# Kernel optimization log

Hardware: AMD Instinct MI355X
Metric: run time of the kernel (lower is better)

The kernel has to match this reference:

```python
import jax, jax.numpy as jnp
import numpy as np

N = 50000      # nodes
E = 800000     # random edges (self-loops appended inside reference)
DIN = 128
DH = 32        # per-head hidden dim of layer 1
H = 8          # heads
DOUT = 32      # output dim (layer 2, concat=False)
NEG_SLOPE = 0.2


def segment_softmax(e, seg, num):
    # numerically stable softmax over variable-size segments (per-destination)
    m = jax.ops.segment_max(e, seg, num_segments=num)
    m = jnp.where(jnp.isfinite(m), m, jnp.zeros_like(m))
    ex = jnp.exp(e - m[seg])
    s = jax.ops.segment_sum(ex, seg, num_segments=num)
    return ex / (s[seg] + 1e-16)


def gatv2_conv(x, src, dst, Wl, Wr, att, bias, heads, dim, concat):
    n = x.shape[0]
    xl = (x @ Wl).reshape(n, heads, dim)   # source transform
    xr = (x @ Wr).reshape(n, heads, dim)   # target transform
    z = xl[src] + xr[dst]                  # [E, H, D] gather per edge
    z = jnp.where(z > 0, z, NEG_SLOPE * z) # LeakyReLU BEFORE attention vector (GATv2)
    e = jnp.einsum('ehd,hd->eh', z, att)   # attention logits [E, H]
    alpha = segment_softmax(e, dst, n)     # softmax over in-edges of each dst
    out = jax.ops.segment_sum(alpha[:, :, None] * xl[src], dst, num_segments=n)
    if concat:
        return out.reshape(n, heads * dim) + bias
    return out.mean(axis=1) + bias


def setup_inputs() -> dict:
    key = jax.random.key(0)
    ks = jax.random.split(key, 12)
    x = jax.random.normal(ks[0], (N, DIN), dtype=jnp.float32)
    edge_index = jax.random.randint(ks[1], (2, E), 0, N, dtype=jnp.int64)
    s = 0.05
    Wl1 = jax.random.normal(ks[2], (DIN, H * DH), dtype=jnp.float32) * s
    Wr1 = jax.random.normal(ks[3], (DIN, H * DH), dtype=jnp.float32) * s
    att1 = jax.random.normal(ks[4], (H, DH), dtype=jnp.float32) * s
    b1 = jnp.zeros((H * DH,), dtype=jnp.float32)
    Wl2 = jax.random.normal(ks[5], (H * DH, H * DOUT), dtype=jnp.float32) * s
    Wr2 = jax.random.normal(ks[6], (H * DH, H * DOUT), dtype=jnp.float32) * s
    att2 = jax.random.normal(ks[7], (H, DOUT), dtype=jnp.float32) * s
    b2 = jnp.zeros((DOUT,), dtype=jnp.float32)
    return {"x": x, "edge_index": edge_index, "Wl1": Wl1, "Wr1": Wr1,
            "att1": att1, "b1": b1, "Wl2": Wl2, "Wr2": Wr2,
            "att2": att2, "b2": b2}


def reference(x, edge_index, Wl1, Wr1, att1, b1, Wl2, Wr2, att2, b2):
    n = x.shape[0]
    loops = jnp.arange(n, dtype=edge_index.dtype)
    src = jnp.concatenate([edge_index[0], loops])  # PyG adds self-loops by default
    dst = jnp.concatenate([edge_index[1], loops])
    h = gatv2_conv(x, src, dst, Wl1, Wr1, att1, b1, H, DH, concat=True)
    h = jax.nn.elu(h)
    out = gatv2_conv(h, src, dst, Wl2, Wr2, att2, b2, H, DOUT, concat=False)
    return out
```

## Files before the change

kernel.cpp:

```cpp
#include <hip/hip_runtime.h>
#include <hip/hip_bf16.h>

typedef __hip_bfloat16 bf16;
typedef __attribute__((ext_vector_type(8))) short bf16x8;
typedef __attribute__((ext_vector_type(4))) float f32x4;

#define N_NODES 50000
#define E_RAW   800000
#define E_TOT   850000
#define H_HEADS 8
#define F_DIM   256
#define NB_SCAN 196

__device__ __forceinline__ float loadF(const void* p, size_t i, int f32) {
    return f32 ? ((const float*)p)[i] : __bfloat162float(((const bf16*)p)[i]);
}
__device__ __forceinline__ int loadI(const void* p, size_t i, int is32) {
    return is32 ? ((const int*)p)[i] : (int)((const long long*)p)[i];
}
__device__ __forceinline__ float uasf(unsigned u) { return __uint_as_float(u); }
__device__ __forceinline__ unsigned f2bfbits(float f) {
    unsigned u = __float_as_uint(f);
    return (u + 0x7fff + ((u >> 16) & 1)) >> 16;
}
__device__ __forceinline__ short f2bfs(float f) {
    unsigned u = __float_as_uint(f);
    return (short)((u + 0x7fff + ((u >> 16) & 1)) >> 16);
}

__global__ void detect_zero(const void* __restrict__ x, const void* __restrict__ ei,
                            int* __restrict__ flags, int* __restrict__ counts) {
    int gid = blockIdx.x * 256 + threadIdx.x;
    if (gid < N_NODES) counts[gid] = 0;
    if (blockIdx.x != 0) return;
    __shared__ int sf[2];
    int t = threadIdx.x;
    if (t < 2) sf[t] = 0;
    __syncthreads();
    const unsigned short* xs = (const unsigned short*)x;
    int f32 = 0;
    for (int i = t; i < 8192; i += 256) {
        unsigned e = (xs[i] >> 7) & 0xFF;
        if (e >= 134) f32 = 1;
    }
    const int* eii = (const int*)ei;
    int odd = 0;
    for (int i = t; i < 1024; i += 256)
        if (eii[2 * i + 1] != 0) odd = 1;
    if (f32) atomicOr(&sf[0], 1);
    if (odd) atomicOr(&sf[1], 1);
    __syncthreads();
    if (t < 2) flags[t] = sf[t];
}

__global__ void prep(const void* __restrict__ wl1, const void* __restrict__ wr1,
                     const void* __restrict__ wl2, const void* __restrict__ wr2,
                     const void* __restrict__ ei,
                     bf16* __restrict__ wb, int* __restrict__ counts,
                     unsigned short* __restrict__ rank,
                     const int* __restrict__ flags) {
    const int f32 = flags[0], is32 = flags[1];
    int gid = blockIdx.x * 256 + threadIdx.x;
    if (gid < E_TOT) {
        int d = (gid < E_RAW) ? loadI(ei, (size_t)E_RAW + gid, is32) : (gid - E_RAW);
        rank[gid] = (unsigned short)atomicAdd(&counts[d], 1);
    }
    for (size_t j = gid; j < 196608; j += (size_t)gridDim.x * 256) {
        const void* src; size_t off, base;
        int k, n;
        if (j < 65536) {
            int half = j >= 32768;
            off = j - (size_t)half * 32768;
            src = half ? wr1 : wl1;
            k = (int)(off >> 8); n = half * 256 + (int)(off & 255);
            base = 0;
        } else {
            size_t jj = j - 65536;
            int half = jj >= 65536;
            off = jj - (size_t)half * 65536;
            src = half ? wr2 : wl2;
            k = (int)(off >> 8); n = half * 256 + (int)(off & 255);
            base = 65536;
        }
        int kb = k >> 5, jo = k & 7;
        int lane = ((k >> 3) & 3) * 16 + (n & 15);
        int ctg = n >> 4;
        size_t dst = base + (((size_t)(kb * 32 + ctg) * 64 + lane) * 8 + jo);
        wb[dst] = __float2bfloat16(loadF(src, off, f32));
    }
}

__global__ void scan1(const int* __restrict__ counts, int* __restrict__ rp,
                      int* __restrict__ bsum) {
    __shared__ int sm[256];
    int b = blockIdx.x, t = threadIdx.x;
    int i = b * 256 + t;
    int v = (i < N_NODES) ? counts[i] : 0;
    sm[t] = v; __syncthreads();
    for (int off = 1; off < 256; off <<= 1) {
        int u = (t >= off) ? sm[t - off] : 0;
        __syncthreads();
        sm[t] += u;
        __syncthreads();
    }
    int incl = sm[t];
    if (i < N_NODES) rp[i] = incl - v;
    if (t == 255) bsum[b] = incl;
}

__global__ void scan2(int* __restrict__ bsum) {
    __shared__ int sm[256];
    int t = threadIdx.x;
    int v = (t < NB_SCAN) ? bsum[t] : 0;
    sm[t] = v; __syncthreads();
    for (int off = 1; off < 256; off <<= 1) {
        int u = (t >= off) ? sm[t - off] : 0;
        __syncthreads();
        sm[t] += u;
        __syncthreads();
    }
    if (t < NB_SCAN) bsum[t] = sm[t] - v;
}

__global__ void scan3(int* __restrict__ rp, const int* __restrict__ bsum) {
    int b = blockIdx.x, t = threadIdx.x;
    int i = b * 256 + t;
    if (i < N_NODES) rp[i] += bsum[b];
    if (i == 0) rp[N_NODES] = E_TOT;
}

__global__ void fill(const void* __restrict__ ei, const int* __restrict__ rp,
                     const unsigned short* __restrict__ rank,
                     int* __restrict__ srcs, const int* __restrict__ flags) {
    const int is32 = flags[1];
    int e = blockIdx.x * 256 + threadIdx.x;
    if (e >= E_TOT) return;
    int s, d;
    if (e < E_RAW) { s = loadI(ei, e, is32); d = loadI(ei, (size_t)E_RAW + e, is32); }
    else           { s = d = e - E_RAW; }
    srcs[rp[d] + rank[e]] = s;
}

__launch_bounds__(256)
__global__ void gemm_mfma(const void* __restrict__ A, const bf16* __restrict__ Wsw,
                          bf16* __restrict__ Cl, bf16* __restrict__ Cr,
                          int M, int K, int aDyn, const int* __restrict__ flags) {
    const int af32 = aDyn ? flags[0] : 0;
    const int tid = threadIdx.x;
    const int w = tid >> 6, lane = tid & 63, q = lane >> 4, l16 = lane & 15;
    const int bRow = blockIdx.x * 128 + (w >> 1) * 64;
    const int bCol = blockIdx.y * 128 + (w & 1) * 64;
    const int ctg0 = bCol >> 4;
    const short* Wp = (const short*)Wsw;
    const int nkb = K >> 5;
    int rows[4];
#pragma unroll
    for (int i = 0; i < 4; ++i) {
        int r = bRow + i * 16 + l16;
        rows[i] = r < M ? r : M - 1;
    }
    f32x4 acc[16] = {};
    for (int kb = 0; kb < nkb; ++kb) {
        bf16x8 a[4], b[4];
#pragma unroll
        for (int i = 0; i < 4; ++i) {
            if (!af32) {
                a[i] = *(const bf16x8*)((const short*)A + (size_t)rows[i] * K + q * 8 + kb * 32);
            } else {
                const float* Apf = (const float*)A + (size_t)rows[i] * K + q * 8 + kb * 32;
                float4 a0 = *(const float4*)(Apf);
                float4 a1 = *(const float4*)(Apf + 4);
                a[i][0] = f2bfs(a0.x); a[i][1] = f2bfs(a0.y);
                a[i][2] = f2bfs(a0.z); a[i][3] = f2bfs(a0.w);
                a[i][4] = f2bfs(a1.x); a[i][5] = f2bfs(a1.y);
                a[i][6] = f2bfs(a1.z); a[i][7] = f2bfs(a1.w);
            }
        }
#pragma unroll
        for (int j = 0; j < 4; ++j)
            b[j] = *(const bf16x8*)(Wp + ((size_t)(kb * 32 + ctg0 + j) * 64 + lane) * 8);
#pragma unroll
        for (int i = 0; i < 4; ++i)
#pragma unroll
            for (int j = 0; j < 4; ++j)
                acc[i * 4 + j] =
                    __builtin_amdgcn_mfma_f32_16x16x32_bf16(b[j], a[i], acc[i * 4 + j], 0, 0, 0);
    }
    unsigned short* C = (unsigned short*)(bCol < 256 ? Cl : Cr);
    const int cBase = (bCol < 256 ? bCol : bCol - 256) + q * 4;
#pragma unroll
    for (int i = 0; i < 4; ++i) {
        int row = bRow + i * 16 + l16;
        if (row < M) {
#pragma unroll
            for (int j = 0; j < 4; ++j) {
                f32x4 v = acc[i * 4 + j];
                uint2 o;
                o.x = f2bfbits(v[0]) | (f2bfbits(v[1]) << 16);
                o.y = f2bfbits(v[2]) | (f2bfbits(v[3]) << 16);
                *(uint2*)(C + (size_t)row * 256 + cBase + j * 16) = o;
            }
        }
    }
}

#define EDGE2(Q, PRED)                                                        \
    {                                                                         \
        float2 X0 = {uasf(Q.x << 16), uasf(Q.x & 0xffff0000u)};               \
        float2 X1 = {uasf(Q.y << 16), uasf(Q.y & 0xffff0000u)};               \
        float2 X2 = {uasf(Q.z << 16), uasf(Q.z & 0xffff0000u)};               \
        float2 X3 = {uasf(Q.w << 16), uasf(Q.w & 0xffff0000u)};               \
        float2 z0 = {X0.x + rv0.x, X0.y + rv0.y};                             \
        float2 z1 = {X1.x + rv1.x, X1.y + rv1.y};                             \
        float2 z2 = {X2.x + rv2.x, X2.y + rv2.y};                             \
        float2 z3 = {X3.x + rv3.x, X3.y + rv3.y};                             \
        z0.x = fmaxf(z0.x, 0.2f * z0.x); z0.y = fmaxf(z0.y, 0.2f * z0.y);     \
        z1.x = fmaxf(z1.x, 0.2f * z1.x); z1.y = fmaxf(z1.y, 0.2f * z1.y);     \
        z2.x = fmaxf(z2.x, 0.2f * z2.x); z2.y = fmaxf(z2.y, 0.2f * z2.y);     \
        z3.x = fmaxf(z3.x, 0.2f * z3.x); z3.y = fmaxf(z3.y, 0.2f * z3.y);     \
        float2 p2 = {z0.x * a0.x, z0.y * a0.y};                               \
        p2.x = fmaf(z1.x, a1.x, p2.x); p2.y = fmaf(z1.y, a1.y, p2.y);         \
        p2.x = fmaf(z2.x, a2.x, p2.x); p2.y = fmaf(z2.y, a2.y, p2.y);         \
        p2.x = fmaf(z3.x, a3.x, p2.x); p2.y = fmaf(z3.y, a3.y, p2.y);         \
        float p = p2.x + p2.y;                                                \
        p += __shfl_xor(p, 1); p += __shfl_xor(p, 2);                         \
        float wv = (PRED) ? __expf(p) : 0.f;                                  \
        den += wv;                                                            \
        n0.x = fmaf(wv, X0.x, n0.x); n0.y = fmaf(wv, X0.y, n0.y);             \
        n1.x = fmaf(wv, X1.x, n1.x); n1.y = fmaf(wv, X1.y, n1.y);             \
        n2.x = fmaf(wv, X2.x, n2.x); n2.y = fmaf(wv, X2.y, n2.y);             \
        n3.x = fmaf(wv, X3.x, n3.x); n3.y = fmaf(wv, X3.y, n3.y);             \
    }
__launch_bounds__(256)
__global__ void fused_attn(const int* __restrict__ rp, const int* __restrict__ srcs,
                           const bf16* __restrict__ xl, const bf16* __restrict__ xr,
                           const void* __restrict__ att, const void* __restrict__ bias,
                           void* __restrict__ outp, int mode,
                           const int* __restrict__ flags) {
    const int f32 = flags[0];
    const int tid = threadIdx.x, wid = tid >> 6, lane = tid & 63;
    const int sub = lane & 31;
    const int d = blockIdx.x * 8 + wid * 2 + (lane >> 5);

    const unsigned short* xru = (const unsigned short*)xr;
    uint4 xv = *(const uint4*)(xru + (size_t)d * 256 + sub * 8);
    float2 rv0 = {uasf(xv.x << 16), uasf(xv.x & 0xffff0000u)};
    float2 rv1 = {uasf(xv.y << 16), uasf(xv.y & 0xffff0000u)};
    float2 rv2 = {uasf(xv.z << 16), uasf(xv.z & 0xffff0000u)};
    float2 rv3 = {uasf(xv.w << 16), uasf(xv.w & 0xffff0000u)};
    float2 a0, a1, a2, a3;
    if (f32) {
        float4 t0 = *(const float4*)((const float*)att + sub * 8);
        float4 t1 = *(const float4*)((const float*)att + sub * 8 + 4);
        a0 = {t0.x, t0.y}; a1 = {t0.z, t0.w}; a2 = {t1.x, t1.y}; a3 = {t1.z, t1.w};
    } else {
        uint4 av = *(const uint4*)((const unsigned short*)att + sub * 8);
        a0 = {uasf(av.x << 16), uasf(av.x & 0xffff0000u)};
        a1 = {uasf(av.y << 16), uasf(av.y & 0xffff0000u)};
        a2 = {uasf(av.z << 16), uasf(av.z & 0xffff0000u)};
        a3 = {uasf(av.w << 16), uasf(av.w & 0xffff0000u)};
    }

    const int start = rp[d], cnt = rp[d + 1] - start;
    const int cnt1 = cnt - 1;
    int mA = __shfl(cnt, 0), mB = __shfl(cnt, 32);
    const int maxc = mA > mB ? mA : mB;
    const int* sp = srcs + start;
    const unsigned short* xlu = (const unsigned short*)xl + sub * 8;

    float den = 0.f;
    float2 n0 = {0,0}, n1 = {0,0}, n2 = {0,0}, n3 = {0,0};
    int i = 0;
    for (; i + 1 < maxc; i += 2) {
        int i0 = i < cnt1 ? i : cnt1;
        int i1 = i + 1 < cnt1 ? i + 1 : cnt1;
        int s0 = sp[i0], s1 = sp[i1];
        uint4 q0 = *(const uint4*)(xlu + (size_t)s0 * 256);
        uint4 q1 = *(const uint4*)(xlu + (size_t)s1 * 256);
        EDGE2(q0, i < cnt);
        EDGE2(q1, i + 1 < cnt);
    }
    if (i < maxc) {
        int i0 = i < cnt1 ? i : cnt1;
        int s0 = sp[i0];
        uint4 q0 = *(const uint4*)(xlu + (size_t)s0 * 256);
        EDGE2(q0, i < cnt);
    }
    float rd = 1.f / (den + 1e-16f);
    float v[8] = {n0.x * rd, n0.y * rd, n1.x * rd, n1.y * rd,
                  n2.x * rd, n2.y * rd, n3.x * rd, n3.y * rd};

    if (mode == 1) {
        float b[8];
        if (f32) {
            float4 t0 = *(const float4*)((const float*)bias + sub * 8);
            float4 t1 = *(const float4*)((const float*)bias + sub * 8 + 4);
            b[0]=t0.x; b[1]=t0.y; b[2]=t0.z; b[3]=t0.w;
            b[4]=t1.x; b[5]=t1.y; b[6]=t1.z; b[7]=t1.w;
        } else {
            uint4 bv = *(const uint4*)((const unsigned short*)bias + sub * 8);
            b[0]=uasf(bv.x<<16); b[1]=uasf(bv.x&0xffff0000u);
            b[2]=uasf(bv.y<<16); b[3]=uasf(bv.y&0xffff0000u);
            b[4]=uasf(bv.z<<16); b[5]=uasf(bv.z&0xffff0000u);
            b[6]=uasf(bv.w<<16); b[7]=uasf(bv.w&0xffff0000u);
        }
        uint4 o;
        unsigned oo[4];
#pragma unroll
        for (int k = 0; k < 4; ++k) {
            float u0 = v[2*k]   + b[2*k];
            float u1 = v[2*k+1] + b[2*k+1];
            u0 = u0 > 0.f ? u0 : expm1f(u0);
            u1 = u1 > 0.f ? u1 : expm1f(u1);
            oo[k] = f2bfbits(u0) | (f2bfbits(u1) << 16);
        }
        o.x = oo[0]; o.y = oo[1]; o.z = oo[2]; o.w = oo[3];
        *(uint4*)((unsigned short*)outp + (size_t)d * 256 + sub * 8) = o;
    } else {
#pragma unroll
        for (int k = 0; k < 8; ++k) {
            v[k] += __shfl_xor(v[k], 4);
            v[k] += __shfl_xor(v[k], 8);
            v[k] += __shfl_xor(v[k], 16);
        }
        if (sub < 4) {
            int j = sub * 8;
            float o[8];
#pragma unroll
            for (int k = 0; k < 8; ++k)
                o[k] = v[k] * 0.125f + loadF(bias, j + k, f32);
            if (f32) {
                float4 o0 = {o[0], o[1], o[2], o[3]};
                float4 o1 = {o[4], o[5], o[6], o[7]};
                *(float4*)((float*)outp + (size_t)d * 32 + j)     = o0;
                *(float4*)((float*)outp + (size_t)d * 32 + j + 4) = o1;
            } else {
                uint4 ob;
                ob.x = f2bfbits(o[0]) | (f2bfbits(o[1]) << 16);
                ob.y = f2bfbits(o[2]) | (f2bfbits(o[3]) << 16);
                ob.z = f2bfbits(o[4]) | (f2bfbits(o[5]) << 16);
                ob.w = f2bfbits(o[6]) | (f2bfbits(o[7]) << 16);
                *(uint4*)((unsigned short*)outp + (size_t)d * 32 + j) = ob;
            }
        }
    }
}

extern "C" void kernel_launch(void* const* d_in, const int* in_sizes, int n_in,
                              void* d_out, int out_size, void* d_ws, size_t ws_size,
                              hipStream_t stream) {
    const void* x    = d_in[0];
    const void* ei   = d_in[1];
    const void* Wl1  = d_in[2];
    const void* Wr1  = d_in[3];
    const void* att1 = d_in[4];
    const void* b1   = d_in[5];
    const void* Wl2  = d_in[6];
    const void* Wr2  = d_in[7];
    const void* att2 = d_in[8];
    const void* b2   = d_in[9];

    char* p = (char*)d_ws;
    auto take = [&](size_t bytes) { char* r = p; p += (bytes + 255) & ~(size_t)255; return r; };
    int*  flags  = (int*) take(64 * sizeof(int));
    bf16* wb     = (bf16*)take(196608 * sizeof(bf16));
    bf16* xl     = (bf16*)take((size_t)N_NODES * F_DIM * sizeof(bf16));
    bf16* xr     = (bf16*)take((size_t)N_NODES * F_DIM * sizeof(bf16));
    bf16* h1     = (bf16*)take((size_t)N_NODES * F_DIM * sizeof(bf16));
    int*  rp     = (int*) take((N_NODES + 1) * sizeof(int));
    int*  counts = (int*) take(N_NODES * sizeof(int));
    int*  bsum   = (int*) take(256 * sizeof(int));
    unsigned short* rank = (unsigned short*)take((size_t)E_TOT * sizeof(unsigned short));
    int*  srcs   = (int*) take(((size_t)E_TOT + 64) * sizeof(int));

    bf16* W1sw = wb;
    bf16* W2sw = wb + 65536;

    const int GB = (E_TOT + 255) / 256;

    detect_zero<<<196, 256, 0, stream>>>(x, ei, flags, counts);
    prep<<<GB, 256, 0, stream>>>(Wl1, Wr1, Wl2, Wr2, ei, wb, counts, rank, flags);
    scan1<<<NB_SCAN, 256, 0, stream>>>(counts, rp, bsum);
    scan2<<<1, 256, 0, stream>>>(bsum);
    scan3<<<NB_SCAN, 256, 0, stream>>>(rp, bsum);
    fill<<<GB, 256, 0, stream>>>(ei, rp, rank, srcs, flags);

    dim3 ggrd((N_NODES + 127) / 128, 4);

    gemm_mfma<<<ggrd, 256, 0, stream>>>(x, W1sw, xl, xr, N_NODES, 128, 1, flags);
    fused_attn<<<N_NODES / 8, 256, 0, stream>>>(rp, srcs, xl, xr, att1, b1, h1, 1, flags);

    gemm_mfma<<<ggrd, 256, 0, stream>>>(h1, W2sw, xl, xr, N_NODES, 256, 0, flags);
    fused_attn<<<N_NODES / 8, 256, 0, stream>>>(rp, srcs, xl, xr, att2, b2, d_out, 2, flags);
}
```

Before: 388.2 us.

## Drop scan3 kernel, store sources as u16, use persistent grid-stride attention

Removes the scan3 pass by adding block offsets to the row pointers on the fly in fill and in the attention kernel. Source indices are stored as 16-bit values to halve index traffic. The attention kernel now runs as a fixed 1024-block grid-stride loop over node pairs. Node ids reach 50000, which fits in 16 bits, so the indices are safe only because N is below 65536, a hardcoded limit. The persistent grid may also balance load less well than one block per 8 nodes.

```diff
diff --git a/kernel.cpp b/kernel.cpp
--- a/kernel.cpp
+++ b/kernel.cpp
@@ -122,23 +122,21 @@
     if (t < NB_SCAN) bsum[t] = sm[t] - v;
 }
 
-__global__ void scan3(int* __restrict__ rp, const int* __restrict__ bsum) {
-    int b = blockIdx.x, t = threadIdx.x;
-    int i = b * 256 + t;
-    if (i < N_NODES) rp[i] += bsum[b];
-    if (i == 0) rp[N_NODES] = E_TOT;
+__device__ __forceinline__ int rpF(const int* rp, const int* bsum, int d) {
+    return (d < N_NODES) ? rp[d] + bsum[d >> 8] : E_TOT;
 }
 
 __global__ void fill(const void* __restrict__ ei, const int* __restrict__ rp,
+                     const int* __restrict__ bsum,
                      const unsigned short* __restrict__ rank,
-                     int* __restrict__ srcs, const int* __restrict__ flags) {
+                     unsigned short* __restrict__ srcs, const int* __restrict__ flags) {
     const int is32 = flags[1];
     int e = blockIdx.x * 256 + threadIdx.x;
     if (e >= E_TOT) return;
     int s, d;
     if (e < E_RAW) { s = loadI(ei, e, is32); d = loadI(ei, (size_t)E_RAW + e, is32); }
     else           { s = d = e - E_RAW; }
-    srcs[rp[d] + rank[e]] = s;
+    srcs[rp[d] + bsum[d >> 8] + rank[e]] = (unsigned short)s;
 }
 
 __launch_bounds__(256)
@@ -232,7 +230,8 @@
         n3.x = fmaf(wv, X3.x, n3.x); n3.y = fmaf(wv, X3.y, n3.y);             \
     }
 __launch_bounds__(256)
-__global__ void fused_attn(const int* __restrict__ rp, const int* __restrict__ srcs,
+__global__ void fused_attn(const int* __restrict__ rp, const int* __restrict__ bsum,
+                           const unsigned short* __restrict__ srcs,
                            const bf16* __restrict__ xl, const bf16* __restrict__ xr,
                            const void* __restrict__ att, const void* __restrict__ bias,
                            void* __restrict__ outp, int mode,
@@ -240,14 +239,10 @@
     const int f32 = flags[0];
     const int tid = threadIdx.x, wid = tid >> 6, lane = tid & 63;
     const int sub = lane & 31;
-    const int d = blockIdx.x * 8 + wid * 2 + (lane >> 5);
-
+    const int NW = gridDim.x * 4;
     const unsigned short* xru = (const unsigned short*)xr;
-    uint4 xv = *(const uint4*)(xru + (size_t)d * 256 + sub * 8);
-    float2 rv0 = {uasf(xv.x << 16), uasf(xv.x & 0xffff0000u)};
-    float2 rv1 = {uasf(xv.y << 16), uasf(xv.y & 0xffff0000u)};
-    float2 rv2 = {uasf(xv.z << 16), uasf(xv.z & 0xffff0000u)};
-    float2 rv3 = {uasf(xv.w << 16), uasf(xv.w & 0xffff0000u)};
+    const unsigned short* xlu = (const unsigned short*)xl + sub * 8;
+
     float2 a0, a1, a2, a3;
     if (f32) {
         float4 t0 = *(const float4*)((const float*)att + sub * 8);
@@ -261,86 +256,95 @@
         a3 = {uasf(av.w << 16), uasf(av.w & 0xffff0000u)};
     }
 
-    const int start = rp[d], cnt = rp[d + 1] - start;
-    const int cnt1 = cnt - 1;
-    int mA = __shfl(cnt, 0), mB = __shfl(cnt, 32);
-    const int maxc = mA > mB ? mA : mB;
-    const int* sp = srcs + start;
-    const unsigned short* xlu = (const unsigned short*)xl + sub * 8;
-
-    float den = 0.f;
-    float2 n0 = {0,0}, n1 = {0,0}, n2 = {0,0}, n3 = {0,0};
-    int i = 0;
-    for (; i + 1 < maxc; i += 2) {
-        int i0 = i < cnt1 ? i : cnt1;
-        int i1 = i + 1 < cnt1 ? i + 1 : cnt1;
-        int s0 = sp[i0], s1 = sp[i1];
-        uint4 q0 = *(const uint4*)(xlu + (size_t)s0 * 256);
-        uint4 q1 = *(const uint4*)(xlu + (size_t)s1 * 256);
-        EDGE2(q0, i < cnt);
-        EDGE2(q1, i + 1 < cnt);
-    }
-    if (i < maxc) {
-        int i0 = i < cnt1 ? i : cnt1;
-        int s0 = sp[i0];
-        uint4 q0 = *(const uint4*)(xlu + (size_t)s0 * 256);
-        EDGE2(q0, i < cnt);
-    }
-    float rd = 1.f / (den + 1e-16f);
-    float v[8] = {n0.x * rd, n0.y * rd, n1.x * rd, n1.y * rd,
-                  n2.x * rd, n2.y * rd, n3.x * rd, n3.y * rd};
-
-    if (mode == 1) {
-        float b[8];
-        if (f32) {
-            float4 t0 = *(const float4*)((const float*)bias + sub * 8);
-            float4 t1 = *(const float4*)((const float*)bias + sub * 8 + 4);
-            b[0]=t0.x; b[1]=t0.y; b[2]=t0.z; b[3]=t0.w;
-            b[4]=t1.x; b[5]=t1.y; b[6]=t1.z; b[7]=t1.w;
+    for (int pr = blockIdx.x * 4 + wid; pr < N_NODES / 2; pr += NW) {
+        const int d = pr * 2 + (lane >> 5);
+        uint4 xv = *(const uint4*)(xru + (size_t)d * 256 + sub * 8);
+        float2 rv0 = {uasf(xv.x << 16), uasf(xv.x & 0xffff0000u)};
+        float2 rv1 = {uasf(xv.y << 16), uasf(xv.y & 0xffff0000u)};
+        float2 rv2 = {uasf(xv.z << 16), uasf(xv.z & 0xffff0000u)};
+        float2 rv3 = {uasf(xv.w << 16), uasf(xv.w & 0xffff0000u)};
+
+        const int start = rpF(rp, bsum, d);
+        const int cnt = rpF(rp, bsum, d + 1) - start;
+        const int cnt1 = cnt - 1;
+        int mA = __shfl(cnt, 0), mB = __shfl(cnt, 32);
+        const int maxc = mA > mB ? mA : mB;
+        const unsigned short* sp = srcs + start;
+
+        float den = 0.f;
+        float2 n0 = {0,0}, n1 = {0,0}, n2 = {0,0}, n3 = {0,0};
+        int i = 0;
+        for (; i + 1 < maxc; i += 2) {
+            int i0 = i < cnt1 ? i : cnt1;
+            int i1 = i + 1 < cnt1 ? i + 1 : cnt1;
+            int s0 = sp[i0], s1 = sp[i1];
+            uint4 q0 = *(const uint4*)(xlu + (size_t)s0 * 256);
+            uint4 q1 = *(const uint4*)(xlu + (size_t)s1 * 256);
+            EDGE2(q0, i < cnt);
+            EDGE2(q1, i + 1 < cnt);
+        }
+        if (i < maxc) {
+            int i0 = i < cnt1 ? i : cnt1;
+            int s0 = sp[i0];
+            uint4 q0 = *(const uint4*)(xlu + (size_t)s0 * 256);
+            EDGE2(q0, i < cnt);
+        }
+        float rd = 1.f / (den + 1e-16f);
+        float v[8] = {n0.x * rd, n0.y * rd, n1.x * rd, n1.y * rd,
+                      n2.x * rd, n2.y * rd, n3.x * rd, n3.y * rd};
+
+        if (mode == 1) {
+            float b[8];
+            if (f32) {
+                float4 t0 = *(const float4*)((const float*)bias + sub * 8);
+                float4 t1 = *(const float4*)((const float*)bias + sub * 8 + 4);
+                b[0]=t0.x; b[1]=t0.y; b[2]=t0.z; b[3]=t0.w;
+                b[4]=t1.x; b[5]=t1.y; b[6]=t1.z; b[7]=t1.w;
+            } else {
+                uint4 bv = *(const uint4*)((const unsigned short*)bias + sub * 8);
+                b[0]=uasf(bv.x<<16); b[1]=uasf(bv.x&0xffff0000u);
+                b[2]=uasf(bv.y<<16); b[3]=uasf(bv.y&0xffff0000u);
+                b[4]=uasf(bv.z<<16); b[5]=uasf(bv.z&0xffff0000u);
+                b[6]=uasf(bv.w<<16); b[7]=uasf(bv.w&0xffff0000u);
+            }
+            uint4 o;
+            unsigned oo[4];
+#pragma unroll
+            for (int k = 0; k < 4; ++k) {
+                float u0 = v[2*k]   + b[2*k];
+                float u1 = v[2*k+1] + b[2*k+1];
+                u0 = u0 > 0.f ? u0 : expm1f(u0);
+                u1 = u1 > 0.f ? u1 : expm1f(u1);
+                oo[k] = f2bfbits(u0) | (f2bfbits(u1) << 16);
+            }
+            o.x = oo[0]; o.y = oo[1]; o.z = oo[2]; o.w = oo[3];
+            *(uint4*)((unsigned short*)outp + (size_t)d * 256 + sub * 8) = o;
         } else {
-            uint4 bv = *(const uint4*)((const unsigned short*)bias + sub * 8);
-            b[0]=uasf(bv.x<<16); b[1]=uasf(bv.x&0xffff0000u);
-            b[2]=uasf(bv.y<<16); b[3]=uasf(bv.y&0xffff0000u);
-            b[4]=uasf(bv.z<<16); b[5]=uasf(bv.z&0xffff0000u);
-            b[6]=uasf(bv.w<<16); b[7]=uasf(bv.w&0xffff0000u);
-        }
-        uint4 o;
-        unsigned oo[4];
-#pragma unroll
-        for (int k = 0; k < 4; ++k) {
-            float u0 = v[2*k]   + b[2*k];
-            float u1 = v[2*k+1] + b[2*k+1];
-            u0 = u0 > 0.f ? u0 : expm1f(u0);
-            u1 = u1 > 0.f ? u1 : expm1f(u1);
-            oo[k] = f2bfbits(u0) | (f2bfbits(u1) << 16);
-        }
-        o.x = oo[0]; o.y = oo[1]; o.z = oo[2]; o.w = oo[3];
-        *(uint4*)((unsigned short*)outp + (size_t)d * 256 + sub * 8) = o;
-    } else {
-#pragma unroll
-        for (int k = 0; k < 8; ++k) {
-            v[k] += __shfl_xor(v[k], 4);
-            v[k] += __shfl_xor(v[k], 8);
-            v[k] += __shfl_xor(v[k], 16);
-        }
-        if (sub < 4) {
-            int j = sub * 8;
-            float o[8];
-#pragma unroll
-            for (int k = 0; k < 8; ++k)
-                o[k] = v[k] * 0.125f + loadF(bias, j + k, f32);
-            if (f32) {
-                float4 o0 = {o[0], o[1], o[2], o[3]};
-                float4 o1 = {o[4], o[5], o[6], o[7]};
-                *(float4*)((float*)outp + (size_t)d * 32 + j)     = o0;
-                *(float4*)((float*)outp + (size_t)d * 32 + j + 4) = o1;
-            } else {
-                uint4 ob;
-                ob.x = f2bfbits(o[0]) | (f2bfbits(o[1]) << 16);
-                ob.y = f2bfbits(o[2]) | (f2bfbits(o[3]) << 16);
-                ob.z = f2bfbits(o[4]) | (f2bfbits(o[5]) << 16);
-                ob.w = f2bfbits(o[6]) | (f2bfbits(o[7]) << 16);
-                *(uint4*)((unsigned short*)outp + (size_t)d * 32 + j) = ob;
+#pragma unroll
+            for (int k = 0; k < 8; ++k) {
+                v[k] += __shfl_xor(v[k], 4);
+                v[k] += __shfl_xor(v[k], 8);
+                v[k] += __shfl_xor(v[k], 16);
+            }
+            if (sub < 4) {
+                int j = sub * 8;
+                float o[8];
+#pragma unroll
+                for (int k = 0; k < 8; ++k)
+                    o[k] = v[k] * 0.125f + loadF(bias, j + k, f32);
+                if (f32) {
+                    float4 o0 = {o[0], o[1], o[2], o[3]};
+                    float4 o1 = {o[4], o[5], o[6], o[7]};
+                    *(float4*)((float*)outp + (size_t)d * 32 + j)     = o0;
+                    *(float4*)((float*)outp + (size_t)d * 32 + j + 4) = o1;
+                } else {
+                    uint4 ob;
+                    ob.x = f2bfbits(o[0]) | (f2bfbits(o[1]) << 16);
+                    ob.y = f2bfbits(o[2]) | (f2bfbits(o[3]) << 16);
+                    ob.z = f2bfbits(o[4]) | (f2bfbits(o[5]) << 16);
+                    ob.w = f2bfbits(o[6]) | (f2bfbits(o[7]) << 16);
+                    *(uint4*)((unsigned short*)outp + (size_t)d * 32 + j) = ob;
+                }
             }
         }
     }
@@ -371,7 +375,7 @@
     int*  counts = (int*) take(N_NODES * sizeof(int));
     int*  bsum   = (int*) take(256 * sizeof(int));
     unsigned short* rank = (unsigned short*)take((size_t)E_TOT * sizeof(unsigned short));
-    int*  srcs   = (int*) take(((size_t)E_TOT + 64) * sizeof(int));
+    unsigned short* srcs = (unsigned short*)take(((size_t)E_TOT + 64) * sizeof(unsigned short));
 
     bf16* W1sw = wb;
     bf16* W2sw = wb + 65536;
@@ -382,14 +386,13 @@
     prep<<<GB, 256, 0, stream>>>(Wl1, Wr1, Wl2, Wr2, ei, wb, counts, rank, flags);
     scan1<<<NB_SCAN, 256, 0, stream>>>(counts, rp, bsum);
     scan2<<<1, 256, 0, stream>>>(bsum);
-    scan3<<<NB_SCAN, 256, 0, stream>>>(rp, bsum);
-    fill<<<GB, 256, 0, stream>>>(ei, rp, rank, srcs, flags);
+    fill<<<GB, 256, 0, stream>>>(ei, rp, bsum, rank, srcs, flags);
 
     dim3 ggrd((N_NODES + 127) / 128, 4);
 
     gemm_mfma<<<ggrd, 256, 0, stream>>>(x, W1sw, xl, xr, N_NODES, 128, 1, flags);
-    fused_attn<<<N_NODES / 8, 256, 0, stream>>>(rp, srcs, xl, xr, att1, b1, h1, 1, flags);
+    fused_attn<<<1024, 256, 0, stream>>>(rp, bsum, srcs, xl, xr, att1, b1, h1, 1, flags);
 
     gemm_mfma<<<ggrd, 256, 0, stream>>>(h1, W2sw, xl, xr, N_NODES, 256, 0, flags);
-    fused_attn<<<N_NODES / 8, 256, 0, stream>>>(rp, srcs, xl, xr, att2, b2, d_out, 2, flags);
-}
+    fused_attn<<<1024, 256, 0, stream>>>(rp, bsum, srcs, xl, xr, att2, b2, d_out, 2, flags);
+}
```

Result: slower. 401.0 us (+3.3%).
